# Kernel optimization log

Measured on AMD Instinct MI355X. Metric: run time of the kernel, lower is better.

The kernel has to match this reference:

```python
import jax, jax.numpy as jnp
import numpy as np

N = 64      # SSM state size (hidden_size)
H = 1024    # channels
L = 2048    # sequence length
BATCH = 8


def setup_inputs() -> dict:
    key = jax.random.key(0)
    ks = jax.random.split(key, 12)
    s = 1.0 / np.sqrt(N)
    n = jnp.arange(N, dtype=jnp.float32)
    return {
        "r": jax.random.normal(ks[0], (BATCH, L, H), dtype=jnp.float32),
        "B_re": jax.random.normal(ks[1], (N,), dtype=jnp.float32) * s,
        "B_im": jax.random.normal(ks[2], (N,), dtype=jnp.float32) * s,
        "C_re": jax.random.normal(ks[3], (H, N), dtype=jnp.float32) * s,
        "C_im": jax.random.normal(ks[4], (H, N), dtype=jnp.float32) * s,
        "P_re": jax.random.normal(ks[5], (N,), dtype=jnp.float32) * s,
        "P_im": jax.random.normal(ks[6], (N,), dtype=jnp.float32) * s,
        "Q_re": jax.random.normal(ks[7], (N,), dtype=jnp.float32) * s,
        "Q_im": jax.random.normal(ks[8], (N,), dtype=jnp.float32) * s,
        # HiPPO-LegS-like diagonal: negative real part for stability, imag ~ pi*n
        "diag_re": -0.5 * jnp.ones((N,), dtype=jnp.float32),
        "diag_im": jnp.pi * (n - N / 2.0),
        "step": jnp.array([1e-3], dtype=jnp.float32),
        "D": jnp.zeros((1,), dtype=jnp.float32),
    }


def _dplr_kernel(Bc, Cc, Pc, Qc, Lam, step, seq_len):
    # Standard S4 DPLR generating function evaluated at roots of unity,
    # then inverse FFT -> real convolution kernel K_c of shape (H, L).
    z = jnp.exp(-2j * jnp.pi * jnp.arange(seq_len) / seq_len).astype(jnp.complex64)  # (L,)
    g = (2.0 / step) * (1.0 - z) / (1.0 + z)                                          # (L,)
    cden = 1.0 / (g[:, None] - Lam[None, :])                                          # (L,N) Cauchy denom
    k00 = jnp.einsum('hn,ln->hl', Cc * Bc, cden)   # (H,L)
    k01 = jnp.einsum('hn,ln->hl', Cc * Pc, cden)   # (H,L)
    k10 = jnp.einsum('n,ln->l', Qc * Bc, cden)     # (L,)
    k11 = jnp.einsum('n,ln->l', Qc * Pc, cden)     # (L,)
    at_roots = (2.0 / (1.0 + z)) * (k00 - k01 * (k10 / (1.0 + k11)))  # (H,L)
    return jnp.fft.ifft(at_roots, axis=-1).real


def reference(r, B_re, B_im, C_re, C_im, P_re, P_im, Q_re, Q_im,
              diag_re, diag_im, step, D):
    step_c = jnp.maximum(step[0], 1e-6)
    Bc = B_re + 1j * B_im
    Cc = C_re + 1j * C_im
    Pc = P_re + 1j * P_im
    Qc = Q_re + 1j * Q_im
    Lam = diag_re + 1j * diag_im
    seq_len = r.shape[1]
    K = _dplr_kernel(Bc, Cc, Pc, Qc, Lam, step_c, seq_len)  # (H, L)
    # causal FFT convolution along the sequence axis
    nfft = 2 * seq_len
    Kf = jnp.fft.rfft(K, n=nfft, axis=-1)            # (H, nfft//2+1)
    uf = jnp.fft.rfft(r, n=nfft, axis=1)             # (B, nfft//2+1, H)
    h1 = jnp.fft.irfft(uf * Kf.T[None], n=nfft, axis=1)[:, :seq_len]  # (B,L,H)
    y1 = h1 + D[0] * r
    return jax.nn.gelu(y1, approximate=False)
```

## Files before the change

### kernel.cpp

```cpp
#include <hip/hip_runtime.h>
#include <math.h>

#define SSM_N 64
#define SSM_H 1024
#define SSM_L 2048
#define SSM_B 8
#define FFTN 2048
#define NT 256
#define KFS 2052

#define PSWZ(a) ((a) ^ (((a) >> 4) & 15))

typedef float f2 __attribute__((ext_vector_type(2)));
static __device__ __forceinline__ f2 mkf2(float a, float b){ f2 v; v.x = a; v.y = b; return v; }

static __device__ __forceinline__ f2 cmul(f2 a, f2 b){
  return mkf2(-a.y, a.y) * mkf2(b.y, b.x) + mkf2(a.x, a.x) * b;
}
static __device__ __forceinline__ f2 cconj(f2 a){ return mkf2(a.x, -a.y); }

template<bool INV> static __device__ __forceinline__ f2 mul_mi(f2 a){
  return INV ? mkf2(-a.y, a.x) : mkf2(a.y, -a.x);
}
template<bool INV> static __device__ __forceinline__ f2 mul_w81(f2 a){
  const float r = 0.70710678118654752440f;
  return INV ? (r * mkf2(a.x - a.y, a.y + a.x)) : (r * mkf2(a.x + a.y, a.y - a.x));
}
template<bool INV> static __device__ __forceinline__ f2 mul_w83(f2 a){
  const float r = 0.70710678118654752440f;
  return INV ? (r * mkf2(-(a.x + a.y), a.x - a.y)) : (r * mkf2(a.y - a.x, -(a.x + a.y)));
}

#define W8C0 1.f
#define W8S0 0.f
#define W8C1 0.92387953251f
#define W8S1 (-0.38268343236f)
#define W8C2 0.70710678119f
#define W8S2 (-0.70710678119f)
#define W8C3 0.38268343236f
#define W8S3 (-0.92387953251f)
#define W8C4 0.f
#define W8S4 (-1.f)
#define W8C5 (-0.38268343236f)
#define W8S5 (-0.92387953251f)
#define W8C6 (-0.70710678119f)
#define W8S6 (-0.70710678119f)
#define W8C7 (-0.92387953251f)
#define W8S7 (-0.38268343236f)

template<bool INV>
static __device__ __forceinline__ void bfly8_store(f2* __restrict__ dst, const f2* __restrict__ tw,
                                                   f2* x, int j, int base, int S)
{
  f2 t0=x[0]+x[4], t4=x[0]-x[4];
  f2 t1=x[1]+x[5], t5=x[1]-x[5];
  f2 t2=x[2]+x[6], t6=x[2]-x[6];
  f2 t3=x[3]+x[7], t7=x[3]-x[7];
  f2 b0=t0+t2, b2=t0-t2, b1=t1+t3, b3=t1-t3;
  f2 mb3 = mul_mi<INV>(b3);
  f2 y0=b0+b1, y4=b0-b1, y2=b2+mb3, y6=b2-mb3;
  f2 v1 = mul_w81<INV>(t5), v2 = mul_mi<INV>(t6), v3 = mul_w83<INV>(t7);
  f2 a0=t4+v2, a2=t4-v2, a1=v1+v3, a3=v1-v3;
  f2 ma3 = mul_mi<INV>(a3);
  f2 y1=a0+a1, y5=a0-a1, y3=a2+ma3, y7=a2-ma3;
  f2 w1 = tw[j];
  if (INV) w1.y = -w1.y;
  f2 w2 = cmul(w1,w1);
  f2 w3 = cmul(w2,w1);
  f2 w4 = cmul(w2,w2);
  f2 w5 = cmul(w3,w2);
  f2 w6 = cmul(w3,w3);
  f2 w7 = cmul(w4,w3);
  dst[PSWZ(base)]     = y0;
  dst[PSWZ(base+S)]   = cmul(y1,w1);
  dst[PSWZ(base+2*S)] = cmul(y2,w2);
  dst[PSWZ(base+3*S)] = cmul(y3,w3);
  dst[PSWZ(base+4*S)] = cmul(y4,w4);
  dst[PSWZ(base+5*S)] = cmul(y5,w5);
  dst[PSWZ(base+6*S)] = cmul(y6,w6);
  dst[PSWZ(base+7*S)] = cmul(y7,w7);
}

template<bool INV, bool ZTOP>
static __device__ __forceinline__ void stage8_first(const f2* __restrict__ src, f2* __restrict__ dst,
                                                    const f2* __restrict__ tw, int t, int st)
{
  const f2* sp = src + st;
  f2 x[8];
  if (ZTOP) {
    #pragma unroll
    for (int q = 0; q < 4; ++q) { x[q] = sp[256*q]; x[q+4] = mkf2(0.f, 0.f); }
  } else {
    #pragma unroll
    for (int q = 0; q < 8; ++q) x[q] = sp[256*q];
  }
  bfly8_store<INV>(dst, tw, x, t, t*8, 1);
}

template<bool INV, int S>
static __device__ __forceinline__ void stage8_mid(const f2* __restrict__ src, f2* __restrict__ dst,
                                                  const f2* __restrict__ tw, int t, int st)
{
  const f2* sp = src + st;
  f2 x[8];
  #pragma unroll
  for (int q = 0; q < 8; ++q) x[q] = sp[256*q];
  int i = t & (S-1);
  int j = t - i;
  bfly8_store<INV>(dst, tw, x, j, i + j*8, S);
}

template<bool INV, bool HALFOUT>
static __device__ __forceinline__ void stage4f(const f2* __restrict__ src, f2* __restrict__ dst, int st)
{
  #pragma unroll
  for (int hh = 0; hh < 2; ++hh) {
    const f2* sp = src + st + 256*hh;
    f2* wp = dst + st + 256*hh;
    f2 x0=sp[0], x1=sp[512], x2=sp[1024], x3=sp[1536];
    f2 a0=x0+x2, a2=x0-x2, a1=x1+x3, a3=x1-x3;
    f2 m = mul_mi<INV>(a3);
    wp[0]   = a0+a1;
    wp[512] = a2+m;
    if (!HALFOUT) {
      wp[1024] = a0-a1;
      wp[1536] = a2-m;
    }
  }
}

template<bool INV, bool ZTOP, bool HALFOUT>
static __device__ void fft2048(f2* A, f2* B, const f2* tw, int t, int st)
{
  __syncthreads();
  stage8_first<INV, ZTOP>(A, B, tw, t, st);
  __syncthreads();
  stage8_mid<INV, 8>(B, A, tw, t, st);
  __syncthreads();
  stage8_mid<INV, 64>(A, B, tw, t, st);
  __syncthreads();
  stage4f<INV, HALFOUT>(B, A, st);
  __syncthreads();
}

static __device__ __forceinline__ void init_tw(f2* tw, int t)
{
  float s, c;
  sincosf(-6.2831853071795864769f * (float)t / (float)FFTN, &s, &c);
  tw[t] = mkf2(c, s);
}

__global__ __launch_bounds__(256) void kernel_cden(
    const float* __restrict__ B_re, const float* __restrict__ B_im,
    const float* __restrict__ P_re, const float* __restrict__ P_im,
    const float* __restrict__ Q_re, const float* __restrict__ Q_im,
    const float* __restrict__ diag_re, const float* __restrict__ diag_im,
    const float* __restrict__ step,
    f2* __restrict__ cdenT, f2* __restrict__ f2v, f2* __restrict__ facv)
{
  int gid = blockIdx.x * blockDim.x + threadIdx.x;
  int l = gid >> 3, s = gid & 7;
  double stepc = (double)step[0]; if (stepc < 1e-6) stepc = 1e-6;
  double ang = -2.0 * 3.14159265358979323846 * (double)l / (double)SSM_L;
  double zr = cos(ang), zi = sin(ang);
  double dr = 1.0 + zr, di = zi;
  double nr = 1.0 - zr, ni = -zi;
  double den = dr*dr + di*di;
  double i2s = 2.0 / stepc;
  double gr = i2s * (nr*dr + ni*di) / den;
  double gi = i2s * (ni*dr - nr*di) / den;
  double k10r=0.0, k10i=0.0, k11r=0.0, k11i=0.0;
  #pragma unroll
  for (int q = 0; q < 8; ++q) {
    int n = s*8 + q;
    double ar = gr - (double)diag_re[n];
    double ai = gi - (double)diag_im[n];
    double d2 = ar*ar + ai*ai;
    double cr = ar/d2, ci = -ai/d2;
    cdenT[n*SSM_L + l] = mkf2((float)cr, (float)ci);
    double qr = (double)Q_re[n], qi = (double)Q_im[n];
    double br = (double)B_re[n], bi = (double)B_im[n];
    double pr = (double)P_re[n], pi = (double)P_im[n];
    double qbr = qr*br - qi*bi, qbi = qr*bi + qi*br;
    double qpr = qr*pr - qi*pi, qpi = qr*pi + qi*pr;
    k10r += qbr*cr - qbi*ci; k10i += qbr*ci + qbi*cr;
    k11r += qpr*cr - qpi*ci; k11i += qpr*ci + qpi*cr;
  }
  #pragma unroll
  for (int off = 1; off < 8; off <<= 1) {
    k10r += __shfl_xor(k10r, off);
    k10i += __shfl_xor(k10i, off);
    k11r += __shfl_xor(k11r, off);
    k11i += __shfl_xor(k11i, off);
  }
  if (s == 0) {
    f2v[l] = mkf2((float)(2.0*dr/den), (float)(-2.0*di/den));
    double er = 1.0 + k11r, ei = k11i;
    double ed = er*er + ei*ei;
    facv[l] = mkf2((float)((k10r*er + k10i*ei)/ed), (float)((k10i*er - k10r*ei)/ed));
  }
}

__global__ __launch_bounds__(NT, 2) void kgemm(
    const float* __restrict__ C_re, const float* __restrict__ C_im,
    const float* __restrict__ B_re, const float* __restrict__ B_im,
    const float* __restrict__ P_re, const float* __restrict__ P_im,
    const f2* __restrict__ cdenT, const f2* __restrict__ f2v, const f2* __restrict__ facv,
    f2* __restrict__ atr)
{
  __shared__ f2 cbs[256];
  int t = threadIdx.x;
  int h0 = blockIdx.x * 2;
  if (t < 128) {
    int h = h0 + (t >> 6), n = t & 63;
    f2 cc = mkf2(C_re[h*SSM_N + n], C_im[h*SSM_N + n]);
    cbs[t]       = cmul(cc, mkf2(B_re[n], B_im[n]));
    cbs[128 + t] = cmul(cc, mkf2(P_re[n], P_im[n]));
  }
  __syncthreads();
  f2 k00[2][8], k01[2][8];
  #pragma unroll
  for (int h = 0; h < 2; ++h)
    #pragma unroll
    for (int i = 0; i < 8; ++i) { k00[h][i] = mkf2(0.f,0.f); k01[h][i] = mkf2(0.f,0.f); }
  for (int n = 0; n < SSM_N; ++n) {
    f2 cd[8];
    #pragma unroll
    for (int i = 0; i < 8; ++i) cd[i] = cdenT[n*SSM_L + t + i*NT];
    #pragma unroll
    for (int h = 0; h < 2; ++h) {
      f2 cb = cbs[h*64 + n], cp = cbs[128 + h*64 + n];
      #pragma unroll
      for (int i = 0; i < 8; ++i) {
        k00[h][i] = k00[h][i] + cmul(cb, cd[i]);
        k01[h][i] = k01[h][i] + cmul(cp, cd[i]);
      }
    }
  }
  #pragma unroll
  for (int h = 0; h < 2; ++h) {
    f2* arow = atr + (size_t)(h0 + h) * SSM_L;
    #pragma unroll
    for (int i = 0; i < 8; ++i) {
      int l = t + i*NT;
      arow[l] = cmul(f2v[l], k00[h][i] - cmul(k01[h][i], facv[l]));
    }
  }
}

__global__ __launch_bounds__(NT, 4) void kfft(const f2* __restrict__ atr, f2* __restrict__ Kf)
{
  __shared__ f2 bufA[FFTN];
  __shared__ f2 bufB[FFTN];
  __shared__ f2 tw[256];
  int t = threadIdx.x;
  int st = PSWZ(t);
  int h = blockIdx.x;
  init_tw(tw, t);
  const f2* arow = atr + (size_t)h * SSM_L;
  #pragma unroll
  for (int i = 0; i < 8; ++i) {
    int n = t + i*NT;
    bufA[PSWZ(n)] = arow[n];
  }
  fft2048<true, false, false>(bufA, bufB, tw, t, st);
  float sb, cb;
  sincosf(-3.14159265358979f * (float)t / (float)FFTN, &sb, &cb);
  f2 base = mkf2(cb, sb);
  const float scale = 1.0f / (float)FFTN;
  {
    const float Wc[8] = {W8C0,W8C1,W8C2,W8C3,W8C4,W8C5,W8C6,W8C7};
    const float Ws[8] = {W8S0,W8S1,W8S2,W8S3,W8S4,W8S5,W8S6,W8S7};
    #pragma unroll
    for (int i = 0; i < 8; ++i) {
      int n = t + i*NT;
      float K = bufA[PSWZ(n)].x * scale;
      f2 c = cmul(base, mkf2(Wc[i], Ws[i]));
      bufB[PSWZ(n)] = K * c;
    }
  }
  fft2048<false, false, true>(bufB, bufA, tw, t, st);
  f2* krow = Kf + (size_t)h * KFS;
  #pragma unroll
  for (int i = 0; i < 4; ++i) {
    int m = t + i*NT;
    krow[2*m+1] = bufB[PSWZ(m)];
  }
  #pragma unroll
  for (int i = 0; i < 4; ++i) {
    int m = t + i*NT;
    if (m == 0) {
      krow[0]    = mkf2(arow[0].x, 0.f);
      krow[FFTN] = mkf2(arow[FFTN/2].x, 0.f);
    } else {
      krow[2*m] = 0.5f * (arow[m] + cconj(arow[FFTN - m]));
    }
  }
}

__global__ __launch_bounds__(256) void ktranspose(const float* __restrict__ src, float* __restrict__ dst)
{
  __shared__ float til[64][65];
  int t = threadIdx.x, tx = t & 15, ty = t >> 4;
  int h0 = blockIdx.x * 64, l0 = blockIdx.y * 64, b = blockIdx.z;
  const float4* s4 = (const float4*)(src + ((size_t)b*SSM_L + l0)*SSM_H + h0);
  #pragma unroll
  for (int i = 0; i < 4; ++i) {
    int lr = ty + 16*i;
    float4 v = s4[(size_t)lr*(SSM_H/4) + tx];
    til[lr][4*tx+0]=v.x; til[lr][4*tx+1]=v.y; til[lr][4*tx+2]=v.z; til[lr][4*tx+3]=v.w;
  }
  __syncthreads();
  float4* d4 = (float4*)(dst + ((size_t)b*SSM_H + h0)*SSM_L + l0);
  #pragma unroll
  for (int i = 0; i < 4; ++i) {
    int hr = ty + 16*i;
    float4 w;
    w.x = til[4*tx+0][hr]; w.y = til[4*tx+1][hr];
    w.z = til[4*tx+2][hr]; w.w = til[4*tx+3][hr];
    d4[(size_t)hr*(SSM_L/4) + tx] = w;
  }
}

__global__ __launch_bounds__(NT, 4) void kernel_conv(float* __restrict__ rT, const f2* __restrict__ Kf,
                                                     const float* __restrict__ Dp)
{
  __shared__ f2 bufA[FFTN];
  __shared__ f2 bufB[FFTN];
  __shared__ f2 tw[256];
  int t = threadIdx.x;
  int st = PSWZ(t);
  int row = blockIdx.x;
  int h = row & (SSM_H - 1);
  float Dv = Dp[0];
  init_tw(tw, t);
  float* rrow = rT + (size_t)row * SSM_L;
  const float4* r4 = (const float4*)rrow;
  float4 vin[2];
  #pragma unroll
  for (int i = 0; i < 2; ++i) {
    int j2 = t + i*NT;
    vin[i] = r4[j2];
    bufA[PSWZ(2*j2)]   = mkf2(vin[i].x, vin[i].y);
    bufA[PSWZ(2*j2+1)] = mkf2(vin[i].z, vin[i].w);
  }
  fft2048<false, true, false>(bufA, bufB, tw, t, st);
  const f2* krow = Kf + (size_t)h * KFS;
  float sb, cb;
  sincosf(-3.14159265358979f * (float)t / (float)FFTN, &sb, &cb);
  f2 base = mkf2(cb, sb);
  {
    const float Wc[4] = {W8C0,W8C1,W8C2,W8C3};
    const float Ws[4] = {W8S0,W8S1,W8S2,W8S3};
    #pragma unroll
    for (int i = 0; i < 4; ++i) {
      int k = t + i*NT;
      f2 w = cmul(base, mkf2(Wc[i], Ws[i]));
      float c = w.x, s = w.y;
      if (k == 0) {
        f2 c0 = bufA[0];
        float F0 = c0.x + c0.y, Fn = c0.x - c0.y;
        f2 K0 = krow[0], Kn = krow[FFTN];
        f2 G0 = F0 * K0;
        f2 Gn = Fn * Kn;
        f2 Xe = 0.5f * (G0 + Gn);
        f2 Xo = 0.5f * (G0 - Gn);
        bufB[0] = mkf2(Xe.x - Xo.y, Xe.y + Xo.x);
        f2 Gm = cmul(cconj(bufA[PSWZ(FFTN/2)]), krow[FFTN/2]);
        bufB[PSWZ(FFTN/2)] = cconj(Gm);
      } else {
        int kk = FFTN - k;
        f2 Ck = bufA[PSWZ(k)], Ckk = bufA[PSWZ(kk)];
        f2 E = mkf2(0.5f*(Ck.x + Ckk.x), 0.5f*(Ck.y - Ckk.y));
        f2 O = mkf2(0.5f*(Ck.y + Ckk.y), 0.5f*(Ckk.x - Ck.x));
        f2 Fk  = E + cmul(mkf2(c, s), O);
        f2 Fkk = cconj(E) + cmul(mkf2(-c, s), cconj(O));
        f2 Gk  = cmul(Fk,  krow[k]);
        f2 Gkk = cmul(Fkk, krow[kk]);
        f2 Xe  = mkf2(0.5f*(Gk.x + Gkk.x), 0.5f*(Gk.y - Gkk.y));
        f2 Dd  = mkf2(0.5f*(Gk.x - Gkk.x), 0.5f*(Gk.y + Gkk.y));
        f2 Xo  = cmul(mkf2(c, -s), Dd);
        bufB[PSWZ(k)] = mkf2(Xe.x - Xo.y, Xe.y + Xo.x);
        f2 Xe2 = mkf2(0.5f*(Gkk.x + Gk.x), 0.5f*(Gkk.y - Gk.y));
        f2 Dd2 = mkf2(0.5f*(Gkk.x - Gk.x), 0.5f*(Gkk.y + Gk.y));
        f2 Xo2 = cmul(mkf2(-c, -s), Dd2);
        bufB[PSWZ(kk)] = mkf2(Xe2.x - Xo2.y, Xe2.y + Xo2.x);
      }
    }
  }
  fft2048<true, false, true>(bufB, bufA, tw, t, st);
  const float sc = 1.0f / (float)FFTN;
  float4* w4 = (float4*)rrow;
  #pragma unroll
  for (int i = 0; i < 2; ++i) {
    int j2 = t + i*NT;
    f2 z0 = bufB[PSWZ(2*j2)], z1 = bufB[PSWZ(2*j2+1)];
    w4[j2] = make_float4(z0.x*sc + Dv*vin[i].x, z0.y*sc + Dv*vin[i].y,
                         z1.x*sc + Dv*vin[i].z, z1.y*sc + Dv*vin[i].w);
  }
}

__global__ __launch_bounds__(256) void ktback(const float* __restrict__ yT, float* __restrict__ out)
{
  __shared__ float til[64][65];
  int t = threadIdx.x, tx = t & 15, ty = t >> 4;
  int h0 = blockIdx.x * 64, l0 = blockIdx.y * 64, b = blockIdx.z;
  const float4* s4 = (const float4*)(yT + ((size_t)b*SSM_H + h0)*SSM_L + l0);
  #pragma unroll
  for (int i = 0; i < 4; ++i) {
    int hr = ty + 16*i;
    float4 v = s4[(size_t)hr*(SSM_L/4) + tx];
    til[hr][4*tx+0]=v.x; til[hr][4*tx+1]=v.y; til[hr][4*tx+2]=v.z; til[hr][4*tx+3]=v.w;
  }
  __syncthreads();
  float4* d4 = (float4*)(out + ((size_t)b*SSM_L + l0)*SSM_H + h0);
  #pragma unroll
  for (int i = 0; i < 4; ++i) {
    int lr = ty + 16*i;
    float4 w;
    float x0 = til[4*tx+0][lr], x1 = til[4*tx+1][lr];
    float x2 = til[4*tx+2][lr], x3 = til[4*tx+3][lr];
    w.x = 0.5f * x0 * (1.0f + erff(x0 * 0.70710678118654752f));
    w.y = 0.5f * x1 * (1.0f + erff(x1 * 0.70710678118654752f));
    w.z = 0.5f * x2 * (1.0f + erff(x2 * 0.70710678118654752f));
    w.w = 0.5f * x3 * (1.0f + erff(x3 * 0.70710678118654752f));
    d4[(size_t)lr*(SSM_H/4) + tx] = w;
  }
}

extern "C" void kernel_launch(void* const* d_in, const int* in_sizes, int n_in,
                              void* d_out, int out_size, void* d_ws, size_t ws_size,
                              hipStream_t stream)
{
  const float* r       = (const float*)d_in[0];
  const float* B_re    = (const float*)d_in[1];
  const float* B_im    = (const float*)d_in[2];
  const float* C_re    = (const float*)d_in[3];
  const float* C_im    = (const float*)d_in[4];
  const float* P_re    = (const float*)d_in[5];
  const float* P_im    = (const float*)d_in[6];
  const float* Q_re    = (const float*)d_in[7];
  const float* Q_im    = (const float*)d_in[8];
  const float* diag_re = (const float*)d_in[9];
  const float* diag_im = (const float*)d_in[10];
  const float* step    = (const float*)d_in[11];
  const float* Dp      = (const float*)d_in[12];
  float* out = (float*)d_out;

  char* p = (char*)d_ws;
  float* rT  = (float*)p; p += (size_t)SSM_B*SSM_H*SSM_L*sizeof(float);
  f2* cdenT  = (f2*)p;    p += (size_t)SSM_N*SSM_L*sizeof(f2);
  f2* f2v    = (f2*)p;    p += (size_t)SSM_L*sizeof(f2);
  f2* facv   = (f2*)p;    p += (size_t)SSM_L*sizeof(f2);
  f2* Kf     = (f2*)p;    p += (size_t)SSM_H*KFS*sizeof(f2);
  f2* atr = (f2*)rT;

  kernel_cden<<<SSM_L*8/NT, NT, 0, stream>>>(B_re, B_im, P_re, P_im, Q_re, Q_im,
                                             diag_re, diag_im, step, cdenT, f2v, facv);
  kgemm<<<SSM_H/2, NT, 0, stream>>>(C_re, C_im, B_re, B_im, P_re, P_im,
                                    cdenT, f2v, facv, atr);
  kfft<<<SSM_H, NT, 0, stream>>>(atr, Kf);
  ktranspose<<<dim3(SSM_H/64, SSM_L/64, SSM_B), 256, 0, stream>>>(r, rT);
  kernel_conv<<<SSM_B*SSM_H, NT, 0, stream>>>(rT, Kf, Dp);
  ktback<<<dim3(SSM_H/64, SSM_L/64, SSM_B), 256, 0, stream>>>(rT, out);
}
```

Measured before the change: 287.3 us.

## Fuse prep kernels, run FFTs in place, and use precomputed twiddle table

Merges the input transpose with the Cauchy-denominator setup into one launch, and fuses the kernel-generating GEMM with its FFT so the intermediate never goes to global memory. The 2048-point FFT now runs in place in a single shared buffer, reading a 1024-entry twiddle table instead of computing twiddle powers by chained complex multiplies. This halves shared memory per convolution block so more blocks fit per CU. The cost is extra barriers per stage, a re-read of the input row from global for the D term, and a serial two-row loop in the fused kernel-generation block.

Result: slower. 319.6 us (+11.2%).

```diff
diff --git a/kernel.cpp b/kernel.cpp
--- a/kernel.cpp
+++ b/kernel.cpp
@@ -21,14 +21,6 @@
 
 template<bool INV> static __device__ __forceinline__ f2 mul_mi(f2 a){
   return INV ? mkf2(-a.y, a.x) : mkf2(a.y, -a.x);
-}
-template<bool INV> static __device__ __forceinline__ f2 mul_w81(f2 a){
-  const float r = 0.70710678118654752440f;
-  return INV ? (r * mkf2(a.x - a.y, a.y + a.x)) : (r * mkf2(a.x + a.y, a.y - a.x));
-}
-template<bool INV> static __device__ __forceinline__ f2 mul_w83(f2 a){
-  const float r = 0.70710678118654752440f;
-  return INV ? (r * mkf2(-(a.x + a.y), a.x - a.y)) : (r * mkf2(a.y - a.x, -(a.x + a.y)));
 }
 
 #define W8C0 1.f
@@ -48,10 +40,39 @@
 #define W8C7 (-0.92387953251f)
 #define W8S7 (-0.38268343236f)
 
-template<bool INV>
-static __device__ __forceinline__ void bfly8_store(f2* __restrict__ dst, const f2* __restrict__ tw,
-                                                   f2* x, int j, int base, int S)
-{
+template<bool INV> static __device__ __forceinline__ f2 twget(const f2* __restrict__ tw, int e){
+  f2 w = tw[e & 1023];
+  w = (e & 1024) ? -w : w;
+  if (INV) w.y = -w.y;
+  return w;
+}
+
+static __device__ __forceinline__ void init_tw1024(f2* tw, int t){
+  #pragma unroll
+  for (int i = 0; i < 4; ++i) {
+    int e = t + 256*i;
+    float s, c;
+    sincosf(-6.2831853071795864769f * (float)e / (float)FFTN, &s, &c);
+    tw[e] = mkf2(c, s);
+  }
+}
+
+template<bool INV, int S, bool ZTOP>
+static __device__ __forceinline__ void stage8_ip(f2* __restrict__ buf, const f2* __restrict__ tw,
+                                                 int t, int st)
+{
+  f2 x[8];
+  {
+    const f2* sp = buf + st;
+    if (ZTOP) {
+      #pragma unroll
+      for (int q = 0; q < 4; ++q) { x[q] = sp[256*q]; x[q+4] = mkf2(0.f, 0.f); }
+    } else {
+      #pragma unroll
+      for (int q = 0; q < 8; ++q) x[q] = sp[256*q];
+    }
+  }
+  __syncthreads();
   f2 t0=x[0]+x[4], t4=x[0]-x[4];
   f2 t1=x[1]+x[5], t5=x[1]-x[5];
   f2 t2=x[2]+x[6], t6=x[2]-x[6];
@@ -59,67 +80,43 @@
   f2 b0=t0+t2, b2=t0-t2, b1=t1+t3, b3=t1-t3;
   f2 mb3 = mul_mi<INV>(b3);
   f2 y0=b0+b1, y4=b0-b1, y2=b2+mb3, y6=b2-mb3;
-  f2 v1 = mul_w81<INV>(t5), v2 = mul_mi<INV>(t6), v3 = mul_w83<INV>(t7);
+  const float r = 0.70710678118654752440f;
+  f2 v1 = INV ? (r * mkf2(t5.x - t5.y, t5.y + t5.x)) : (r * mkf2(t5.x + t5.y, t5.y - t5.x));
+  f2 v2 = mul_mi<INV>(t6);
+  f2 v3 = INV ? (r * mkf2(-(t7.x + t7.y), t7.x - t7.y)) : (r * mkf2(t7.y - t7.x, -(t7.x + t7.y)));
   f2 a0=t4+v2, a2=t4-v2, a1=v1+v3, a3=v1-v3;
   f2 ma3 = mul_mi<INV>(a3);
   f2 y1=a0+a1, y5=a0-a1, y3=a2+ma3, y7=a2-ma3;
-  f2 w1 = tw[j];
-  if (INV) w1.y = -w1.y;
-  f2 w2 = cmul(w1,w1);
-  f2 w3 = cmul(w2,w1);
-  f2 w4 = cmul(w2,w2);
-  f2 w5 = cmul(w3,w2);
-  f2 w6 = cmul(w3,w3);
-  f2 w7 = cmul(w4,w3);
-  dst[PSWZ(base)]     = y0;
-  dst[PSWZ(base+S)]   = cmul(y1,w1);
-  dst[PSWZ(base+2*S)] = cmul(y2,w2);
-  dst[PSWZ(base+3*S)] = cmul(y3,w3);
-  dst[PSWZ(base+4*S)] = cmul(y4,w4);
-  dst[PSWZ(base+5*S)] = cmul(y5,w5);
-  dst[PSWZ(base+6*S)] = cmul(y6,w6);
-  dst[PSWZ(base+7*S)] = cmul(y7,w7);
-}
-
-template<bool INV, bool ZTOP>
-static __device__ __forceinline__ void stage8_first(const f2* __restrict__ src, f2* __restrict__ dst,
-                                                    const f2* __restrict__ tw, int t, int st)
-{
-  const f2* sp = src + st;
-  f2 x[8];
-  if (ZTOP) {
-    #pragma unroll
-    for (int q = 0; q < 4; ++q) { x[q] = sp[256*q]; x[q+4] = mkf2(0.f, 0.f); }
-  } else {
-    #pragma unroll
-    for (int q = 0; q < 8; ++q) x[q] = sp[256*q];
-  }
-  bfly8_store<INV>(dst, tw, x, t, t*8, 1);
-}
-
-template<bool INV, int S>
-static __device__ __forceinline__ void stage8_mid(const f2* __restrict__ src, f2* __restrict__ dst,
-                                                  const f2* __restrict__ tw, int t, int st)
-{
-  const f2* sp = src + st;
-  f2 x[8];
-  #pragma unroll
-  for (int q = 0; q < 8; ++q) x[q] = sp[256*q];
   int i = t & (S-1);
   int j = t - i;
-  bfly8_store<INV>(dst, tw, x, j, i + j*8, S);
+  int base = i + j*8;
+  buf[PSWZ(base)]     = y0;
+  buf[PSWZ(base+S)]   = cmul(y1, twget<INV>(tw, j));
+  buf[PSWZ(base+2*S)] = cmul(y2, twget<INV>(tw, 2*j));
+  buf[PSWZ(base+3*S)] = cmul(y3, twget<INV>(tw, 3*j));
+  buf[PSWZ(base+4*S)] = cmul(y4, twget<INV>(tw, 4*j));
+  buf[PSWZ(base+5*S)] = cmul(y5, twget<INV>(tw, 5*j));
+  buf[PSWZ(base+6*S)] = cmul(y6, twget<INV>(tw, 6*j));
+  buf[PSWZ(base+7*S)] = cmul(y7, twget<INV>(tw, 7*j));
+  __syncthreads();
 }
 
 template<bool INV, bool HALFOUT>
-static __device__ __forceinline__ void stage4f(const f2* __restrict__ src, f2* __restrict__ dst, int st)
-{
+static __device__ __forceinline__ void stage4_ip(f2* __restrict__ buf, int st)
+{
+  f2 x[2][4];
   #pragma unroll
   for (int hh = 0; hh < 2; ++hh) {
-    const f2* sp = src + st + 256*hh;
-    f2* wp = dst + st + 256*hh;
-    f2 x0=sp[0], x1=sp[512], x2=sp[1024], x3=sp[1536];
-    f2 a0=x0+x2, a2=x0-x2, a1=x1+x3, a3=x1-x3;
+    const f2* sp = buf + st + 256*hh;
+    x[hh][0]=sp[0]; x[hh][1]=sp[512]; x[hh][2]=sp[1024]; x[hh][3]=sp[1536];
+  }
+  __syncthreads();
+  #pragma unroll
+  for (int hh = 0; hh < 2; ++hh) {
+    f2 a0=x[hh][0]+x[hh][2], a2=x[hh][0]-x[hh][2];
+    f2 a1=x[hh][1]+x[hh][3], a3=x[hh][1]-x[hh][3];
     f2 m = mul_mi<INV>(a3);
+    f2* wp = buf + st + 256*hh;
     wp[0]   = a0+a1;
     wp[512] = a2+m;
     if (!HALFOUT) {
@@ -127,30 +124,21 @@
       wp[1536] = a2-m;
     }
   }
+  __syncthreads();
 }
 
 template<bool INV, bool ZTOP, bool HALFOUT>
-static __device__ void fft2048(f2* A, f2* B, const f2* tw, int t, int st)
-{
-  __syncthreads();
-  stage8_first<INV, ZTOP>(A, B, tw, t, st);
-  __syncthreads();
-  stage8_mid<INV, 8>(B, A, tw, t, st);
-  __syncthreads();
-  stage8_mid<INV, 64>(A, B, tw, t, st);
-  __syncthreads();
-  stage4f<INV, HALFOUT>(B, A, st);
-  __syncthreads();
-}
-
-static __device__ __forceinline__ void init_tw(f2* tw, int t)
-{
-  float s, c;
-  sincosf(-6.2831853071795864769f * (float)t / (float)FFTN, &s, &c);
-  tw[t] = mkf2(c, s);
-}
-
-__global__ __launch_bounds__(256) void kernel_cden(
+static __device__ void fft_ip(f2* buf, const f2* tw, int t, int st)
+{
+  __syncthreads();
+  stage8_ip<INV, 1, ZTOP>(buf, tw, t, st);
+  stage8_ip<INV, 8, false>(buf, tw, t, st);
+  stage8_ip<INV, 64, false>(buf, tw, t, st);
+  stage4_ip<INV, HALFOUT>(buf, st);
+}
+
+__global__ __launch_bounds__(256) void kprep(
+    const float* __restrict__ r, float* __restrict__ rT,
     const float* __restrict__ B_re, const float* __restrict__ B_im,
     const float* __restrict__ P_re, const float* __restrict__ P_im,
     const float* __restrict__ Q_re, const float* __restrict__ Q_im,
@@ -158,59 +146,88 @@
     const float* __restrict__ step,
     f2* __restrict__ cdenT, f2* __restrict__ f2v, f2* __restrict__ facv)
 {
-  int gid = blockIdx.x * blockDim.x + threadIdx.x;
-  int l = gid >> 3, s = gid & 7;
-  double stepc = (double)step[0]; if (stepc < 1e-6) stepc = 1e-6;
-  double ang = -2.0 * 3.14159265358979323846 * (double)l / (double)SSM_L;
-  double zr = cos(ang), zi = sin(ang);
-  double dr = 1.0 + zr, di = zi;
-  double nr = 1.0 - zr, ni = -zi;
-  double den = dr*dr + di*di;
-  double i2s = 2.0 / stepc;
-  double gr = i2s * (nr*dr + ni*di) / den;
-  double gi = i2s * (ni*dr - nr*di) / den;
-  double k10r=0.0, k10i=0.0, k11r=0.0, k11i=0.0;
-  #pragma unroll
-  for (int q = 0; q < 8; ++q) {
-    int n = s*8 + q;
-    double ar = gr - (double)diag_re[n];
-    double ai = gi - (double)diag_im[n];
-    double d2 = ar*ar + ai*ai;
-    double cr = ar/d2, ci = -ai/d2;
-    cdenT[n*SSM_L + l] = mkf2((float)cr, (float)ci);
-    double qr = (double)Q_re[n], qi = (double)Q_im[n];
-    double br = (double)B_re[n], bi = (double)B_im[n];
-    double pr = (double)P_re[n], pi = (double)P_im[n];
-    double qbr = qr*br - qi*bi, qbi = qr*bi + qi*br;
-    double qpr = qr*pr - qi*pi, qpi = qr*pi + qi*pr;
-    k10r += qbr*cr - qbi*ci; k10i += qbr*ci + qbi*cr;
-    k11r += qpr*cr - qpi*ci; k11i += qpr*ci + qpi*cr;
-  }
-  #pragma unroll
-  for (int off = 1; off < 8; off <<= 1) {
-    k10r += __shfl_xor(k10r, off);
-    k10i += __shfl_xor(k10i, off);
-    k11r += __shfl_xor(k11r, off);
-    k11i += __shfl_xor(k11i, off);
-  }
-  if (s == 0) {
-    f2v[l] = mkf2((float)(2.0*dr/den), (float)(-2.0*di/den));
-    double er = 1.0 + k11r, ei = k11i;
-    double ed = er*er + ei*ei;
-    facv[l] = mkf2((float)((k10r*er + k10i*ei)/ed), (float)((k10i*er - k10r*ei)/ed));
-  }
-}
-
-__global__ __launch_bounds__(NT, 2) void kgemm(
+  __shared__ float til[64][65];
+  int bid = blockIdx.x;
+  int t = threadIdx.x;
+  if (bid < 4096) {
+    int tx = t & 15, ty = t >> 4;
+    int h0 = (bid & 15) * 64, l0 = ((bid >> 4) & 31) * 64, b = bid >> 9;
+    const float4* s4 = (const float4*)(r + ((size_t)b*SSM_L + l0)*SSM_H + h0);
+    #pragma unroll
+    for (int i = 0; i < 4; ++i) {
+      int lr = ty + 16*i;
+      float4 v = s4[(size_t)lr*(SSM_H/4) + tx];
+      til[lr][4*tx+0]=v.x; til[lr][4*tx+1]=v.y; til[lr][4*tx+2]=v.z; til[lr][4*tx+3]=v.w;
+    }
+    __syncthreads();
+    float4* d4 = (float4*)(rT + ((size_t)b*SSM_H + h0)*SSM_L + l0);
+    #pragma unroll
+    for (int i = 0; i < 4; ++i) {
+      int hr = ty + 16*i;
+      float4 w;
+      w.x = til[4*tx+0][hr]; w.y = til[4*tx+1][hr];
+      w.z = til[4*tx+2][hr]; w.w = til[4*tx+3][hr];
+      d4[(size_t)hr*(SSM_L/4) + tx] = w;
+    }
+  } else {
+    int gid = (bid - 4096) * 256 + t;
+    int l = gid >> 3, s = gid & 7;
+    double stepc = (double)step[0]; if (stepc < 1e-6) stepc = 1e-6;
+    double ang = -2.0 * 3.14159265358979323846 * (double)l / (double)SSM_L;
+    double zr = cos(ang), zi = sin(ang);
+    double dr = 1.0 + zr, di = zi;
+    double nr = 1.0 - zr, ni = -zi;
+    double den = dr*dr + di*di;
+    double i2s = 2.0 / stepc;
+    double gr = i2s * (nr*dr + ni*di) / den;
+    double gi = i2s * (ni*dr - nr*di) / den;
+    double k10r=0.0, k10i=0.0, k11r=0.0, k11i=0.0;
+    #pragma unroll
+    for (int q = 0; q < 8; ++q) {
+      int n = s*8 + q;
+      double ar = gr - (double)diag_re[n];
+      double ai = gi - (double)diag_im[n];
+      double d2 = ar*ar + ai*ai;
+      double cr = ar/d2, ci = -ai/d2;
+      cdenT[n*SSM_L + l] = mkf2((float)cr, (float)ci);
+      double qr = (double)Q_re[n], qi = (double)Q_im[n];
+      double br = (double)B_re[n], bi = (double)B_im[n];
+      double pr = (double)P_re[n], pi = (double)P_im[n];
+      double qbr = qr*br - qi*bi, qbi = qr*bi + qi*br;
+      double qpr = qr*pr - qi*pi, qpi = qr*pi + qi*pr;
+      k10r += qbr*cr - qbi*ci; k10i += qbr*ci + qbi*cr;
+      k11r += qpr*cr - qpi*ci; k11i += qpr*ci + qpi*cr;
+    }
+    #pragma unroll
+    for (int off = 1; off < 8; off <<= 1) {
+      k10r += __shfl_xor(k10r, off);
+      k10i += __shfl_xor(k10i, off);
+      k11r += __shfl_xor(k11r, off);
+      k11i += __shfl_xor(k11i, off);
+    }
+    if (s == 0) {
+      f2v[l] = mkf2((float)(2.0*dr/den), (float)(-2.0*di/den));
+      double er = 1.0 + k11r, ei = k11i;
+      double ed = er*er + ei*ei;
+      facv[l] = mkf2((float)((k10r*er + k10i*ei)/ed), (float)((k10i*er - k10r*ei)/ed));
+    }
+  }
+}
+
+__global__ __launch_bounds__(NT, 2) void kkern(
     const float* __restrict__ C_re, const float* __restrict__ C_im,
     const float* __restrict__ B_re, const float* __restrict__ B_im,
     const float* __restrict__ P_re, const float* __restrict__ P_im,
     const f2* __restrict__ cdenT, const f2* __restrict__ f2v, const f2* __restrict__ facv,
-    f2* __restrict__ atr)
-{
-  __shared__ f2 cbs[256];
-  int t = threadIdx.x;
+    f2* __restrict__ Kf)
+{
+  __shared__ f2 bufA[FFTN];
+  __shared__ f2 bufB[FFTN];
+  __shared__ f2 tw[1024];
+  int t = threadIdx.x, st = PSWZ(t);
   int h0 = blockIdx.x * 2;
+  init_tw1024(tw, t);
+  f2* cbs = bufA;
   if (t < 128) {
     int h = h0 + (t >> 6), n = t & 63;
     f2 cc = mkf2(C_re[h*SSM_N + n], C_im[h*SSM_N + n]);
@@ -237,118 +254,79 @@
       }
     }
   }
-  #pragma unroll
-  for (int h = 0; h < 2; ++h) {
-    f2* arow = atr + (size_t)(h0 + h) * SSM_L;
-    #pragma unroll
-    for (int i = 0; i < 8; ++i) {
-      int l = t + i*NT;
-      arow[l] = cmul(f2v[l], k00[h][i] - cmul(k01[h][i], facv[l]));
-    }
-  }
-}
-
-__global__ __launch_bounds__(NT, 4) void kfft(const f2* __restrict__ atr, f2* __restrict__ Kf)
-{
-  __shared__ f2 bufA[FFTN];
-  __shared__ f2 bufB[FFTN];
-  __shared__ f2 tw[256];
-  int t = threadIdx.x;
-  int st = PSWZ(t);
-  int h = blockIdx.x;
-  init_tw(tw, t);
-  const f2* arow = atr + (size_t)h * SSM_L;
+  __syncthreads();
   #pragma unroll
   for (int i = 0; i < 8; ++i) {
-    int n = t + i*NT;
-    bufA[PSWZ(n)] = arow[n];
-  }
-  fft2048<true, false, false>(bufA, bufB, tw, t, st);
+    int l = t + i*NT;
+    f2 fv = f2v[l], fc = facv[l];
+    bufA[PSWZ(l)] = cmul(fv, k00[0][i] - cmul(k01[0][i], fc));
+    bufB[PSWZ(l)] = cmul(fv, k00[1][i] - cmul(k01[1][i], fc));
+  }
+  __syncthreads();
+  const float Wc8[8] = {W8C0,W8C1,W8C2,W8C3,W8C4,W8C5,W8C6,W8C7};
+  const float Ws8[8] = {W8S0,W8S1,W8S2,W8S3,W8S4,W8S5,W8S6,W8S7};
   float sb, cb;
   sincosf(-3.14159265358979f * (float)t / (float)FFTN, &sb, &cb);
-  f2 base = mkf2(cb, sb);
-  const float scale = 1.0f / (float)FFTN;
-  {
-    const float Wc[8] = {W8C0,W8C1,W8C2,W8C3,W8C4,W8C5,W8C6,W8C7};
-    const float Ws[8] = {W8S0,W8S1,W8S2,W8S3,W8S4,W8S5,W8S6,W8S7};
+  f2 cbase = mkf2(cb, sb);
+  for (int hh = 0; hh < 2; ++hh) {
+    f2* buf = hh ? bufB : bufA;
+    f2* krow = Kf + (size_t)(h0 + hh) * KFS;
+    #pragma unroll
+    for (int i = 0; i < 4; ++i) {
+      int m = t + i*NT;
+      if (m == 0) {
+        krow[0]    = mkf2(buf[0].x, 0.f);
+        krow[FFTN] = mkf2(buf[PSWZ(FFTN/2)].x, 0.f);
+      } else {
+        krow[2*m] = 0.5f * (buf[PSWZ(m)] + cconj(buf[PSWZ(FFTN - m)]));
+      }
+    }
+    fft_ip<true, false, false>(buf, tw, t, st);
+    f2 tv[8];
+    const float scale = 1.0f / (float)FFTN;
     #pragma unroll
     for (int i = 0; i < 8; ++i) {
       int n = t + i*NT;
-      float K = bufA[PSWZ(n)].x * scale;
-      f2 c = cmul(base, mkf2(Wc[i], Ws[i]));
-      bufB[PSWZ(n)] = K * c;
-    }
-  }
-  fft2048<false, false, true>(bufB, bufA, tw, t, st);
-  f2* krow = Kf + (size_t)h * KFS;
-  #pragma unroll
-  for (int i = 0; i < 4; ++i) {
-    int m = t + i*NT;
-    krow[2*m+1] = bufB[PSWZ(m)];
-  }
-  #pragma unroll
-  for (int i = 0; i < 4; ++i) {
-    int m = t + i*NT;
-    if (m == 0) {
-      krow[0]    = mkf2(arow[0].x, 0.f);
-      krow[FFTN] = mkf2(arow[FFTN/2].x, 0.f);
-    } else {
-      krow[2*m] = 0.5f * (arow[m] + cconj(arow[FFTN - m]));
-    }
-  }
-}
-
-__global__ __launch_bounds__(256) void ktranspose(const float* __restrict__ src, float* __restrict__ dst)
-{
-  __shared__ float til[64][65];
-  int t = threadIdx.x, tx = t & 15, ty = t >> 4;
-  int h0 = blockIdx.x * 64, l0 = blockIdx.y * 64, b = blockIdx.z;
-  const float4* s4 = (const float4*)(src + ((size_t)b*SSM_L + l0)*SSM_H + h0);
-  #pragma unroll
-  for (int i = 0; i < 4; ++i) {
-    int lr = ty + 16*i;
-    float4 v = s4[(size_t)lr*(SSM_H/4) + tx];
-    til[lr][4*tx+0]=v.x; til[lr][4*tx+1]=v.y; til[lr][4*tx+2]=v.z; til[lr][4*tx+3]=v.w;
-  }
-  __syncthreads();
-  float4* d4 = (float4*)(dst + ((size_t)b*SSM_H + h0)*SSM_L + l0);
-  #pragma unroll
-  for (int i = 0; i < 4; ++i) {
-    int hr = ty + 16*i;
-    float4 w;
-    w.x = til[4*tx+0][hr]; w.y = til[4*tx+1][hr];
-    w.z = til[4*tx+2][hr]; w.w = til[4*tx+3][hr];
-    d4[(size_t)hr*(SSM_L/4) + tx] = w;
-  }
-}
-
-__global__ __launch_bounds__(NT, 4) void kernel_conv(float* __restrict__ rT, const f2* __restrict__ Kf,
-                                                     const float* __restrict__ Dp)
-{
-  __shared__ f2 bufA[FFTN];
-  __shared__ f2 bufB[FFTN];
-  __shared__ f2 tw[256];
-  int t = threadIdx.x;
-  int st = PSWZ(t);
+      float K = buf[PSWZ(n)].x * scale;
+      tv[i] = K * cmul(cbase, mkf2(Wc8[i], Ws8[i]));
+    }
+    __syncthreads();
+    #pragma unroll
+    for (int i = 0; i < 8; ++i) buf[PSWZ(t + i*NT)] = tv[i];
+    fft_ip<false, false, true>(buf, tw, t, st);
+    #pragma unroll
+    for (int i = 0; i < 4; ++i) {
+      int m = t + i*NT;
+      krow[2*m+1] = buf[PSWZ(m)];
+    }
+  }
+}
+
+__global__ __launch_bounds__(NT, 6) void kconv(float* __restrict__ rT, const f2* __restrict__ Kf,
+                                               const float* __restrict__ Dp)
+{
+  __shared__ f2 buf[FFTN];
+  __shared__ f2 tw[1024];
+  int t = threadIdx.x, st = PSWZ(t);
   int row = blockIdx.x;
   int h = row & (SSM_H - 1);
   float Dv = Dp[0];
-  init_tw(tw, t);
+  init_tw1024(tw, t);
   float* rrow = rT + (size_t)row * SSM_L;
   const float4* r4 = (const float4*)rrow;
-  float4 vin[2];
   #pragma unroll
   for (int i = 0; i < 2; ++i) {
     int j2 = t + i*NT;
-    vin[i] = r4[j2];
-    bufA[PSWZ(2*j2)]   = mkf2(vin[i].x, vin[i].y);
-    bufA[PSWZ(2*j2+1)] = mkf2(vin[i].z, vin[i].w);
-  }
-  fft2048<false, true, false>(bufA, bufB, tw, t, st);
+    float4 v = r4[j2];
+    buf[PSWZ(2*j2)]   = mkf2(v.x, v.y);
+    buf[PSWZ(2*j2+1)] = mkf2(v.z, v.w);
+  }
+  fft_ip<false, true, false>(buf, tw, t, st);
   const f2* krow = Kf + (size_t)h * KFS;
   float sb, cb;
   sincosf(-3.14159265358979f * (float)t / (float)FFTN, &sb, &cb);
   f2 base = mkf2(cb, sb);
+  f2 outk[4], outkk[4];
   {
     const float Wc[4] = {W8C0,W8C1,W8C2,W8C3};
     const float Ws[4] = {W8S0,W8S1,W8S2,W8S3};
@@ -358,19 +336,17 @@
       f2 w = cmul(base, mkf2(Wc[i], Ws[i]));
       float c = w.x, s = w.y;
       if (k == 0) {
-        f2 c0 = bufA[0];
+        f2 c0 = buf[0];
         float F0 = c0.x + c0.y, Fn = c0.x - c0.y;
-        f2 K0 = krow[0], Kn = krow[FFTN];
-        f2 G0 = F0 * K0;
-        f2 Gn = Fn * Kn;
+        f2 G0 = F0 * krow[0];
+        f2 Gn = Fn * krow[FFTN];
         f2 Xe = 0.5f * (G0 + Gn);
         f2 Xo = 0.5f * (G0 - Gn);
-        bufB[0] = mkf2(Xe.x - Xo.y, Xe.y + Xo.x);
-        f2 Gm = cmul(cconj(bufA[PSWZ(FFTN/2)]), krow[FFTN/2]);
-        bufB[PSWZ(FFTN/2)] = cconj(Gm);
+        outk[0]  = mkf2(Xe.x - Xo.y, Xe.y + Xo.x);
+        outkk[0] = cconj(cmul(cconj(buf[PSWZ(FFTN/2)]), krow[FFTN/2]));
       } else {
         int kk = FFTN - k;
-        f2 Ck = bufA[PSWZ(k)], Ckk = bufA[PSWZ(kk)];
+        f2 Ck = buf[PSWZ(k)], Ckk = buf[PSWZ(kk)];
         f2 E = mkf2(0.5f*(Ck.x + Ckk.x), 0.5f*(Ck.y - Ckk.y));
         f2 O = mkf2(0.5f*(Ck.y + Ckk.y), 0.5f*(Ckk.x - Ck.x));
         f2 Fk  = E + cmul(mkf2(c, s), O);
@@ -380,23 +356,31 @@
         f2 Xe  = mkf2(0.5f*(Gk.x + Gkk.x), 0.5f*(Gk.y - Gkk.y));
         f2 Dd  = mkf2(0.5f*(Gk.x - Gkk.x), 0.5f*(Gk.y + Gkk.y));
         f2 Xo  = cmul(mkf2(c, -s), Dd);
-        bufB[PSWZ(k)] = mkf2(Xe.x - Xo.y, Xe.y + Xo.x);
+        outk[i] = mkf2(Xe.x - Xo.y, Xe.y + Xo.x);
         f2 Xe2 = mkf2(0.5f*(Gkk.x + Gk.x), 0.5f*(Gkk.y - Gk.y));
         f2 Dd2 = mkf2(0.5f*(Gkk.x - Gk.x), 0.5f*(Gkk.y + Gk.y));
         f2 Xo2 = cmul(mkf2(-c, -s), Dd2);
-        bufB[PSWZ(kk)] = mkf2(Xe2.x - Xo2.y, Xe2.y + Xo2.x);
+        outkk[i] = mkf2(Xe2.x - Xo2.y, Xe2.y + Xo2.x);
       }
     }
   }
-  fft2048<true, false, true>(bufB, bufA, tw, t, st);
+  __syncthreads();
+  #pragma unroll
+  for (int i = 0; i < 4; ++i) {
+    int k = t + i*NT;
+    if (k == 0) { buf[0] = outk[0]; buf[PSWZ(FFTN/2)] = outkk[0]; }
+    else        { buf[PSWZ(k)] = outk[i]; buf[PSWZ(FFTN - k)] = outkk[i]; }
+  }
+  fft_ip<true, false, true>(buf, tw, t, st);
   const float sc = 1.0f / (float)FFTN;
   float4* w4 = (float4*)rrow;
   #pragma unroll
   for (int i = 0; i < 2; ++i) {
     int j2 = t + i*NT;
-    f2 z0 = bufB[PSWZ(2*j2)], z1 = bufB[PSWZ(2*j2+1)];
-    w4[j2] = make_float4(z0.x*sc + Dv*vin[i].x, z0.y*sc + Dv*vin[i].y,
-                         z1.x*sc + Dv*vin[i].z, z1.y*sc + Dv*vin[i].w);
+    float4 v = r4[j2];
+    f2 z0 = buf[PSWZ(2*j2)], z1 = buf[PSWZ(2*j2+1)];
+    w4[j2] = make_float4(z0.x*sc + Dv*v.x, z0.y*sc + Dv*v.y,
+                         z1.x*sc + Dv*v.z, z1.y*sc + Dv*v.w);
   }
 }
 
@@ -453,14 +437,11 @@
   f2* f2v    = (f2*)p;    p += (size_t)SSM_L*sizeof(f2);
   f2* facv   = (f2*)p;    p += (size_t)SSM_L*sizeof(f2);
   f2* Kf     = (f2*)p;    p += (size_t)SSM_H*KFS*sizeof(f2);
-  f2* atr = (f2*)rT;
-
-  kernel_cden<<<SSM_L*8/NT, NT, 0, stream>>>(B_re, B_im, P_re, P_im, Q_re, Q_im,
-                                             diag_re, diag_im, step, cdenT, f2v, facv);
-  kgemm<<<SSM_H/2, NT, 0, stream>>>(C_re, C_im, B_re, B_im, P_re, P_im,
-                                    cdenT, f2v, facv, atr);
-  kfft<<<SSM_H, NT, 0, stream>>>(atr, Kf);
-  ktranspose<<<dim3(SSM_H/64, SSM_L/64, SSM_B), 256, 0, stream>>>(r, rT);
-  kernel_conv<<<SSM_B*SSM_H, NT, 0, stream>>>(rT, Kf, Dp);
+
+  kprep<<<4096 + 64, 256, 0, stream>>>(r, rT, B_re, B_im, P_re, P_im, Q_re, Q_im,
+                                       diag_re, diag_im, step, cdenT, f2v, facv);
+  kkern<<<SSM_H/2, NT, 0, stream>>>(C_re, C_im, B_re, B_im, P_re, P_im,
+                                    cdenT, f2v, facv, Kf);
+  kconv<<<SSM_B*SSM_H, NT, 0, stream>>>(rT, Kf, Dp);
   ktback<<<dim3(SSM_H/64, SSM_L/64, SSM_B), 256, 0, stream>>>(rT, out);
 }
```
